# Optimization experiments

Hardware: AMD Instinct MI355X
Metric: run time of the kernel (lower is better)

The kernel has to match this reference:

```python
import math
import jax, jax.numpy as jnp
import numpy as np

N_HEAD = 16
ROPE_BASE = 10000.0


def _rope_tables(T, half, dtype):
    # build_sin_cos(seq_len, dim=head_dim//2): inv freq of length `half`
    pos = jnp.arange(T, dtype=jnp.float32)[:, None]                       # (T,1)
    inv = jnp.exp(jnp.arange(0, 2 * half, 2, dtype=jnp.float32) * (-math.log(ROPE_BASE) / (2 * half)))
    ang = pos * inv                                                        # (T, half)
    return jnp.sin(ang).astype(dtype), jnp.cos(ang).astype(dtype)


def _apply_rope(q, k, sin, cos):
    # q,k: (B,T,H,Dh); sin,cos: (T, Dh//2) -> broadcast over batch and heads
    half = q.shape[-1] // 2
    s = sin[None, :, None, :]
    c = cos[None, :, None, :]
    q1, q2 = q[..., :half], q[..., half:]
    k1, k2 = k[..., :half], k[..., half:]
    q = jnp.concatenate([q1 * c - q2 * s, q2 * c + q1 * s], axis=-1)
    k = jnp.concatenate([k1 * c - k2 * s, k2 * c + k1 * s], axis=-1)
    return q, k


def setup_inputs() -> dict:
    key = jax.random.key(0)
    k1, k2, k3 = jax.random.split(key, 3)
    B, T, C = 2, 2048, 2048
    x = jax.random.normal(k1, (B, T, C), dtype=jnp.float32)
    w_qkv = jax.random.normal(k2, (3 * C, C), dtype=jnp.float32) * (1.0 / math.sqrt(C))
    w_proj = jax.random.normal(k3, (C, C), dtype=jnp.float32) * (1.0 / math.sqrt(C))
    return {"x": x, "w_qkv": w_qkv, "w_proj": w_proj}


def reference(x, w_qkv, w_proj):
    B, T, C = x.shape
    H = N_HEAD
    Dh = C // H
    # fused QKV projection (Linear, no bias): (B,T,3C) -> (B,T,3,H,Dh)
    qkv = jnp.einsum('btc,oc->bto', x, w_qkv).reshape(B, T, 3, H, Dh)
    q, k, v = qkv[:, :, 0], qkv[:, :, 1], qkv[:, :, 2]          # (B,T,H,Dh)
    sin, cos = _rope_tables(T, Dh // 2, x.dtype)
    q, k = _apply_rope(q, k, sin, cos)
    # causal attention, scale 1/sqrt(Dh) (flash default softmax_scale=None)
    scale = 1.0 / math.sqrt(Dh)
    scores = jnp.einsum('bqhd,bkhd->bhqk', q, k) * scale        # (B,H,T,T)
    mask = jnp.tril(jnp.ones((T, T), dtype=bool))
    scores = jnp.where(mask[None, None], scores, jnp.finfo(scores.dtype).min)
    probs = jax.nn.softmax(scores, axis=-1)
    out = jnp.einsum('bhqk,bkhd->bqhd', probs, v)               # (B,T,H,Dh)
    # faithful to original: permute(0,2,1,3) then reshape_as(x)
    out = jnp.transpose(out, (0, 2, 1, 3)).reshape(B, T, C)
    return jnp.einsum('btc,oc->bto', out, w_proj)
```

## Files before the change

kernel.cpp:

```cpp
#include <hip/hip_runtime.h>
#include <hip/hip_bf16.h>

typedef __bf16 bf16_t;
typedef __bf16 bf16x8 __attribute__((ext_vector_type(8)));
typedef float f32x4 __attribute__((ext_vector_type(4)));

#define MFMA16(a, b, c) __builtin_amdgcn_mfma_f32_16x16x32_bf16(a, b, c, 0, 0, 0)

__device__ __forceinline__ void async_copy16(const void* g, void* l) {
  __builtin_amdgcn_global_load_lds(
      (const __attribute__((address_space(1))) void*)g,
      (__attribute__((address_space(3))) void*)l, 16, 0, 0);
}

__global__ void cast_f32_bf16(const float* __restrict__ in, bf16_t* __restrict__ out, int n8) {
  int stride = gridDim.x * blockDim.x;
  for (int i = blockIdx.x * blockDim.x + threadIdx.x; i < n8; i += stride) {
    const float* p = in + (size_t)i * 8;
    f32x4 a = *(const f32x4*)p;
    f32x4 b = *(const f32x4*)(p + 4);
    bf16x8 o;
    o[0] = (bf16_t)a[0]; o[1] = (bf16_t)a[1]; o[2] = (bf16_t)a[2]; o[3] = (bf16_t)a[3];
    o[4] = (bf16_t)b[0]; o[5] = (bf16_t)b[1]; o[6] = (bf16_t)b[2]; o[7] = (bf16_t)b[3];
    *(bf16x8*)(out + (size_t)i * 8) = o;
  }
}

__global__ __launch_bounds__(512, 2) void gemm_qkv(
    const bf16_t* __restrict__ A, const bf16_t* __restrict__ Bw,
    bf16_t* __restrict__ qo, bf16_t* __restrict__ ko,
    int K) {
  __shared__ __align__(16) char lds[131072];
  int tid = threadIdx.x;
  int w = tid >> 6, lane = tid & 63;
  int wm = w & 1, wn = w >> 1;
  int mr = lane & 15, kg = lane >> 4;

  int orig = blockIdx.x;
  int chunk = orig & 7, i = orig >> 3;
  int by = (chunk & 3) * 4 + (i & 3);
  int bx = (chunk >> 2) * 8 + (i >> 2);
  int row0 = by * 256, col0 = bx * 256;

  int lr = tid >> 3, ch = (tid & 7) ^ (lr & 7);
  size_t aoff[4], boff[4];
#pragma unroll
  for (int g = 0; g < 4; ++g) {
    int gr = g * 32 + (lr & 31) + (lr >> 5) * 128;
    aoff[g] = (size_t)(row0 + gr) * K + ch * 8;
  }
#pragma unroll
  for (int p = 0; p < 4; ++p) {
    int gr = (lr >> 4) * 64 + p * 16 + (lr & 15);
    boff[p] = (size_t)(col0 + gr) * K + ch * 8;
  }

  auto stgA = [&](int q, int g, int kt) {
    async_copy16(A + aoff[g] + kt * 64, lds + q * 65536 + g * 8192 + tid * 16);
  };
  auto stgB = [&](int q, int p, int kt) {
    async_copy16(Bw + boff[p] + kt * 64, lds + q * 65536 + 32768 + p * 8192 + tid * 16);
  };

  f32x4 zero = {0.f, 0.f, 0.f, 0.f};
  f32x4 acc[8][4];
#pragma unroll
  for (int mi = 0; mi < 8; ++mi)
#pragma unroll
    for (int ni = 0; ni < 4; ++ni) acc[mi][ni] = zero;

  int nt = K >> 6;

  stgB(0, 0, 0); stgB(0, 1, 0); stgB(0, 2, 0); stgB(0, 3, 0);
  stgA(0, 0, 0); stgA(0, 1, 0); stgA(0, 2, 0); stgA(0, 3, 0);
  asm volatile("s_waitcnt vmcnt(0)" ::: "memory");
  __builtin_amdgcn_sched_barrier(0);
  __builtin_amdgcn_s_barrier();
  __builtin_amdgcn_sched_barrier(0);

#pragma unroll 1
  for (int t = 0; t < nt; ++t) {
    int q = t & 1, qn = q ^ 1;
    int kt = (t + 1 < nt) ? (t + 1) : t;
    const char* Ab = lds + q * 65536;
    const char* Bb = Ab + 32768;
    bf16x8 bf[4][2];

#define QKV_PHASE(MI0, STG0, STG1, WAIT)                                        \
    {                                                                           \
      int r0 = ((MI0) >> 1) * 64 + wm * 32 + mr;                                \
      int r1 = r0 + 16;                                                         \
      bf16x8 a00 = *(const bf16x8*)(Ab + r0 * 128 + ((kg * 16) ^ ((r0 & 7) << 4)));      \
      bf16x8 a01 = *(const bf16x8*)(Ab + r0 * 128 + ((64 + kg * 16) ^ ((r0 & 7) << 4))); \
      bf16x8 a10 = *(const bf16x8*)(Ab + r1 * 128 + ((kg * 16) ^ ((r1 & 7) << 4)));      \
      bf16x8 a11 = *(const bf16x8*)(Ab + r1 * 128 + ((64 + kg * 16) ^ ((r1 & 7) << 4))); \
      STG0; STG1;                                                               \
      __builtin_amdgcn_sched_barrier(0);                                        \
      asm volatile("s_waitcnt vmcnt(" #WAIT ")" ::: "memory");                  \
      __builtin_amdgcn_s_barrier();                                             \
      asm volatile("s_waitcnt lgkmcnt(0)" ::: "memory");                        \
      __builtin_amdgcn_sched_barrier(0);                                        \
      __builtin_amdgcn_s_setprio(1);                                            \
      _Pragma("unroll")                                                         \
      for (int ni = 0; ni < 4; ++ni) {                                          \
        acc[MI0][ni] = MFMA16(a00, bf[ni][0], acc[MI0][ni]);                    \
        acc[MI0][ni] = MFMA16(a01, bf[ni][1], acc[MI0][ni]);                    \
        acc[(MI0) + 1][ni] = MFMA16(a10, bf[ni][0], acc[(MI0) + 1][ni]);        \
        acc[(MI0) + 1][ni] = MFMA16(a11, bf[ni][1], acc[(MI0) + 1][ni]);        \
      }                                                                         \
      __builtin_amdgcn_s_setprio(0);                                            \
      __builtin_amdgcn_sched_barrier(0);                                        \
      __builtin_amdgcn_s_barrier();                                             \
      __builtin_amdgcn_sched_barrier(0);                                        \
    }

#pragma unroll
    for (int ni = 0; ni < 4; ++ni) {
      int rb = ni * 64 + wn * 16 + mr;
      bf[ni][0] = *(const bf16x8*)(Bb + rb * 128 + ((kg * 16) ^ ((rb & 7) << 4)));
      bf[ni][1] = *(const bf16x8*)(Bb + rb * 128 + ((64 + kg * 16) ^ ((rb & 7) << 4)));
    }
    QKV_PHASE(0, stgB(qn, 0, kt), stgB(qn, 1, kt), 4)
    QKV_PHASE(2, stgB(qn, 2, kt), stgB(qn, 3, kt), 5)
    QKV_PHASE(4, stgA(qn, 0, kt), stgA(qn, 1, kt), 6)
    QKV_PHASE(6, stgA(qn, 2, kt), stgA(qn, 3, kt), 3)
#undef QKV_PHASE
  }
  asm volatile("s_waitcnt vmcnt(0)" ::: "memory");
  __syncthreads();

  char* tb = &lds[0];
  int s = col0 >> 11;
  int h0 = (col0 >> 7) & 15;
  int b = row0 >> 11, t0 = row0 & 2047;
#pragma unroll
  for (int mi = 0; mi < 8; ++mi)
#pragma unroll
    for (int ni = 0; ni < 4; ++ni)
#pragma unroll
      for (int jj = 0; jj < 4; ++jj) {
        int rl = wm * 128 + mi * 16 + kg * 4 + jj;
        int cb = (wn * 64 + ni * 16 + mr) * 2;
        *(bf16_t*)(tb + rl * 512 + (cb ^ ((rl & 7) << 4))) = (bf16_t)acc[mi][ni][jj];
      }
  __syncthreads();
  int r = tid >> 1, hs = tid & 1;
  const char* rowb = tb + r * 512;
  int sz = (r & 7) << 4;
  int t = t0 + r;
  bf16_t* dst = (s == 0 ? qo : ko) + ((size_t)((b * 16 + h0 + hs) * 2048 + t)) * 128;
  float tf = (float)t;
  const float cinv = -0.20762050593046014f;
  float postm = (s == 0) ? 0.12751744f : 1.0f;
  bf16x8 vin[16];
#pragma unroll
  for (int m = 0; m < 16; ++m)
    vin[m] = *(const bf16x8*)(rowb + ((hs * 256 + m * 16) ^ sz));
#pragma unroll
  for (int m = 0; m < 8; ++m) {
    bf16x8 o1, o2;
#pragma unroll
    for (int e = 0; e < 8; ++e) {
      float ang = tf * exp2f((float)(m * 8 + e) * cinv);
      float sv = __sinf(ang), cv = __cosf(ang);
      float x1 = (float)vin[m][e], x2 = (float)vin[m + 8][e];
      o1[e] = (bf16_t)((x1 * cv - x2 * sv) * postm);
      o2[e] = (bf16_t)((x2 * cv + x1 * sv) * postm);
    }
    *(bf16x8*)(dst + m * 8) = o1;
    *(bf16x8*)(dst + 64 + m * 8) = o2;
  }
}

template <int MODE>
__global__ __launch_bounds__(512, 2) void gemm256(
    const bf16_t* __restrict__ A, const bf16_t* __restrict__ Bw, float* __restrict__ C,
    bf16_t* __restrict__ vto, int M, int N, int K, int nby, int colbase) {
  __shared__ __align__(16) char lds[147456];
  int tid = threadIdx.x;
  int w = tid >> 6, lane = tid & 63;
  int wm = w >> 1, wn = w & 1;
  int mr = lane & 15, kg = lane >> 4;

  int nwg = gridDim.x;
  int orig = blockIdx.x;
  int wgid = (orig & 7) * (nwg >> 3) + (orig >> 3);
  int by = wgid % nby, bx = wgid / nby;
  int row0 = by * 256, col0 = colbase + bx * 128;

  size_t aoff[4], boff[2];
#pragma unroll
  for (int it = 0; it < 4; ++it) {
    int c = tid + it * 512;
    int r = c >> 3;
    int chs = (c & 7) ^ (r & 7);
    aoff[it] = (size_t)(row0 + r) * K + chs * 8;
  }
#pragma unroll
  for (int it = 0; it < 2; ++it) {
    int c = tid + it * 512;
    int r = c >> 3;
    int chs = (c & 7) ^ (r & 7);
    boff[it] = (size_t)(col0 - colbase + r) * K + chs * 8;
  }

  auto stageA = [&](int buf, int kt, int half) {
    char* Ad = &lds[buf * 49152];
#pragma unroll
    for (int it = half * 2; it < half * 2 + 2; ++it)
      async_copy16(A + aoff[it] + kt * 64, Ad + (tid + it * 512) * 16);
  };
  auto stageB = [&](int buf, int kt) {
    char* Bd = &lds[buf * 49152 + 32768];
#pragma unroll
    for (int it = 0; it < 2; ++it)
      async_copy16(Bw + boff[it] + kt * 64, Bd + (tid + it * 512) * 16);
  };

  f32x4 zero = {0.f, 0.f, 0.f, 0.f};
  f32x4 acc[4][4];
#pragma unroll
  for (int mi = 0; mi < 4; ++mi)
#pragma unroll
    for (int ni = 0; ni < 4; ++ni) acc[mi][ni] = zero;

  int nt = K >> 6;
  stageA(0, 0, 0); stageA(0, 0, 1); stageB(0, 0);
  stageA(1, 1, 0); stageA(1, 1, 1); stageB(1, 1);
  asm volatile("s_waitcnt vmcnt(6)" ::: "memory");
  __builtin_amdgcn_sched_barrier(0);
  __builtin_amdgcn_s_barrier();
  __builtin_amdgcn_sched_barrier(0);

#pragma unroll 1
  for (int t = 0; t < nt; ++t) {
    int cur = t % 3;
    int nxt = (t + 2) % 3;
    int kt2 = (t + 2 < nt) ? (t + 2) : t;
    const char* Ab = &lds[cur * 49152];
    const char* Bb = &lds[cur * 49152 + 32768];
    bf16x8 af[4][2], bfr[4][2];
#pragma unroll
    for (int mi = 0; mi < 4; ++mi) {
      int row = wm * 64 + mi * 16 + mr;
      const char* rb = Ab + row * 128;
      int sz = (row & 7) << 4;
      af[mi][0] = *(const bf16x8*)(rb + ((kg * 16) ^ sz));
      af[mi][1] = *(const bf16x8*)(rb + ((64 + kg * 16) ^ sz));
    }
#pragma unroll
    for (int ni = 0; ni < 4; ++ni) {
      int row = wn * 64 + ni * 16 + mr;
      const char* rb = Bb + row * 128;
      int sz = (row & 7) << 4;
      bfr[ni][0] = *(const bf16x8*)(rb + ((kg * 16) ^ sz));
      bfr[ni][1] = *(const bf16x8*)(rb + ((64 + kg * 16) ^ sz));
    }
    stageA(nxt, kt2, 0);
    __builtin_amdgcn_s_setprio(1);
#pragma unroll
    for (int mi = 0; mi < 4; ++mi) {
      acc[mi][0] = MFMA16(af[mi][0], bfr[0][0], acc[mi][0]);
      acc[mi][0] = MFMA16(af[mi][1], bfr[0][1], acc[mi][0]);
    }
    __builtin_amdgcn_s_setprio(0);
    stageA(nxt, kt2, 1);
    __builtin_amdgcn_s_setprio(1);
#pragma unroll
    for (int mi = 0; mi < 4; ++mi) {
      acc[mi][1] = MFMA16(af[mi][0], bfr[1][0], acc[mi][1]);
      acc[mi][1] = MFMA16(af[mi][1], bfr[1][1], acc[mi][1]);
    }
    __builtin_amdgcn_s_setprio(0);
    stageB(nxt, kt2);
    __builtin_amdgcn_s_setprio(1);
#pragma unroll
    for (int mi = 0; mi < 4; ++mi) {
      acc[mi][2] = MFMA16(af[mi][0], bfr[2][0], acc[mi][2]);
      acc[mi][2] = MFMA16(af[mi][1], bfr[2][1], acc[mi][2]);
      acc[mi][3] = MFMA16(af[mi][0], bfr[3][0], acc[mi][3]);
      acc[mi][3] = MFMA16(af[mi][1], bfr[3][1], acc[mi][3]);
    }
    __builtin_amdgcn_s_setprio(0);
    asm volatile("s_waitcnt vmcnt(6)" ::: "memory");
    __builtin_amdgcn_sched_barrier(0);
    __builtin_amdgcn_s_barrier();
    __builtin_amdgcn_sched_barrier(0);
  }
  asm volatile("s_waitcnt vmcnt(0)" ::: "memory");
  __syncthreads();

  if (MODE == 0) {
#pragma unroll
    for (int mi = 0; mi < 4; ++mi)
#pragma unroll
      for (int ni = 0; ni < 4; ++ni)
#pragma unroll
        for (int jj = 0; jj < 4; ++jj) {
          int row = row0 + wm * 64 + mi * 16 + kg * 4 + jj;
          int col = col0 + wn * 64 + ni * 16 + mr;
          C[(size_t)row * N + col] = acc[mi][ni][jj];
        }
  } else {
    char* tb = &lds[0];
    int h = (col0 >> 7) & 15;
    int b = row0 >> 11, t0 = row0 & 2047;
#pragma unroll
    for (int mi = 0; mi < 4; ++mi)
#pragma unroll
      for (int ni = 0; ni < 4; ++ni)
#pragma unroll
        for (int jj = 0; jj < 4; ++jj) {
          int rloc = wm * 64 + mi * 16 + kg * 4 + jj;
          int cloc = wn * 64 + ni * 16 + mr;
          *(bf16_t*)(tb + cloc * 512 + ((rloc * 2) ^ ((cloc & 7) << 4))) =
              (bf16_t)acc[mi][ni][jj];
        }
    __syncthreads();
    int d = tid >> 2, qt = tid & 3;
    const char* rowb = tb + d * 512;
    int sz = (d & 7) << 4;
    bf16_t* dst = vto + ((size_t)((b * 16 + h) * 128 + d)) * 2048 + t0 + qt * 64;
#pragma unroll
    for (int m2 = 0; m2 < 8; ++m2)
      *(bf16x8*)(dst + m2 * 8) = *(const bf16x8*)(rowb + ((qt * 128 + m2 * 16) ^ sz));
  }
}

__global__ __launch_bounds__(256, 4) void attn_kernel(
    const bf16_t* __restrict__ qg, const bf16_t* __restrict__ kgl,
    const bf16_t* __restrict__ vtg, bf16_t* __restrict__ og) {
  __shared__ __align__(16) bf16_t Ks[64 * 128];
  __shared__ __align__(16) bf16_t Vs[128 * 64];
  __shared__ __align__(16) bf16_t plds[4][1024];
  const int T = 2048;
  int tid = threadIdx.x;
  int w = tid >> 6, lane = tid & 63;
  int mr = lane & 15, kg = lane >> 4;
  int swz = (mr & 7) << 4;

  int L = blockIdx.x;
  int xcd = L & 7, idx = L >> 3;
  int bh = xcd * 4 + (idx & 3);
  int qb = 31 - (idx >> 2);

  const bf16_t* Q = qg + (size_t)bh * T * 128;
  const bf16_t* K = kgl + (size_t)bh * T * 128;
  const bf16_t* Vt = vtg + (size_t)bh * 128 * T;

  int sb = tid * 16;
  int krl = sb >> 8;
  int kc = (sb & 255) ^ ((krl & 7) << 4);
  size_t ksrc = (size_t)krl * 128 + (kc >> 1);
  int vdl = sb >> 7;
  int vc = (sb & 127) ^ ((vdl & 7) << 4);
  size_t vsrc = (size_t)vdl * 2048 + (vc >> 1);

  auto stage = [&](int kb) {
#pragma unroll
    for (int it = 0; it < 4; ++it)
      async_copy16(K + (size_t)(kb + it * 16) * 128 + ksrc, &Ks[it * 2048 + tid * 8]);
#pragma unroll
    for (int it = 0; it < 4; ++it)
      async_copy16(Vt + (size_t)it * 65536 + kb + vsrc, &Vs[it * 2048 + tid * 8]);
  };

  f32x4 zero = {0.f, 0.f, 0.f, 0.f};
  bf16_t* P = &plds[w][0];
  int b = bh >> 4, h = bh & 15;

  int qr0 = qb * 64 + w * 16;
  bf16x8 qf[4];
#pragma unroll
  for (int db = 0; db < 4; ++db)
    qf[db] = *(const bf16x8*)(Q + (size_t)(qr0 + mr) * 128 + db * 32 + kg * 8);

  f32x4 acc[8];
#pragma unroll
  for (int d2 = 0; d2 < 8; ++d2) acc[d2] = zero;
  float mrun[4] = {-1e30f, -1e30f, -1e30f, -1e30f};
  float lpart[4] = {0.f, 0.f, 0.f, 0.f};

  int nj = qb + 1;
#pragma unroll 1
  for (int j = 0; j < nj; ++j) {
    __syncthreads();
    stage(j * 64);
    asm volatile("s_waitcnt vmcnt(0)" ::: "memory");
    __builtin_amdgcn_sched_barrier(0);
    __syncthreads();
    const char* KsB = (const char*)&Ks[0];
    const char* VsB = (const char*)&Vs[0];
    int kb = j * 64;
    f32x4 s[4];
    __builtin_amdgcn_s_setprio(1);
#pragma unroll
    for (int ntl = 0; ntl < 4; ++ntl) {
      s[ntl] = zero;
      int rowb = (ntl * 16 + mr) * 256;
#pragma unroll
      for (int db = 0; db < 4; ++db) {
        bf16x8 kf = *(const bf16x8*)(KsB + rowb + ((db * 64 + kg * 16) ^ swz));
        s[ntl] = MFMA16(qf[db], kf, s[ntl]);
      }
    }
    __builtin_amdgcn_s_setprio(0);
    float pvv[4][4];
    float lmax[4] = {-3e38f, -3e38f, -3e38f, -3e38f};
    bool diag = (j == qb);
#pragma unroll
    for (int ntl = 0; ntl < 4; ++ntl)
#pragma unroll
      for (int jj = 0; jj < 4; ++jj) {
        float v = s[ntl][jj];
        if (diag && (kb + ntl * 16 + mr) > (qr0 + kg * 4 + jj)) v = -1e30f;
        pvv[ntl][jj] = v;
        lmax[jj] = fmaxf(lmax[jj], v);
      }
    bool ok = true;
#pragma unroll
    for (int jj = 0; jj < 4; ++jj) ok &= (lmax[jj] <= mrun[jj] + 8.0f);
    if (!__all(ok)) {
      float tmax[4];
#pragma unroll
      for (int jj = 0; jj < 4; ++jj) tmax[jj] = lmax[jj];
#pragma unroll
      for (int m = 1; m < 16; m <<= 1)
#pragma unroll
        for (int jj = 0; jj < 4; ++jj)
          tmax[jj] = fmaxf(tmax[jj], __shfl_xor(tmax[jj], m, 64));
#pragma unroll
      for (int jj = 0; jj < 4; ++jj) {
        float mn = fmaxf(mrun[jj], tmax[jj]);
        float corr = __builtin_amdgcn_exp2f(mrun[jj] - mn);
        mrun[jj] = mn;
        lpart[jj] *= corr;
#pragma unroll
        for (int d2 = 0; d2 < 8; ++d2) acc[d2][jj] *= corr;
      }
    }
#pragma unroll
    for (int ntl = 0; ntl < 4; ++ntl)
#pragma unroll
      for (int jj = 0; jj < 4; ++jj) {
        float p = __builtin_amdgcn_exp2f(pvv[ntl][jj] - mrun[jj]);
        pvv[ntl][jj] = p;
        lpart[jj] += p;
      }
#pragma unroll
    for (int ntl = 0; ntl < 4; ++ntl)
#pragma unroll
      for (int jj = 0; jj < 4; ++jj) {
        int rr = kg * 4 + jj;
        int cbyte = (mr + ntl * 16) * 2;
        *(bf16_t*)((char*)P + rr * 128 + (cbyte ^ ((rr & 7) << 4))) = (bf16_t)pvv[ntl][jj];
      }
    __builtin_amdgcn_s_setprio(1);
#pragma unroll
    for (int ks = 0; ks < 2; ++ks) {
      int cb = (ks * 32 + kg * 8) * 2;
      bf16x8 pa = *(const bf16x8*)((const char*)P + mr * 128 + (cb ^ ((mr & 7) << 4)));
#pragma unroll
      for (int d2 = 0; d2 < 8; ++d2) {
        bf16x8 vf = *(const bf16x8*)(VsB + (d2 * 16 + mr) * 128 + ((ks * 64 + kg * 16) ^ swz));
        acc[d2] = MFMA16(pa, vf, acc[d2]);
      }
    }
    __builtin_amdgcn_s_setprio(0);
  }
#pragma unroll
  for (int m = 1; m < 16; m <<= 1)
#pragma unroll
    for (int jj = 0; jj < 4; ++jj) lpart[jj] += __shfl_xor(lpart[jj], m, 64);
#pragma unroll
  for (int jj = 0; jj < 4; ++jj) {
    float invl = 1.0f / lpart[jj];
    int t = qr0 + kg * 4 + jj;
    size_t row = (size_t)b * 2048 + h * 128 + (t >> 4);
    bf16_t* orow = og + row * 2048 + (t & 15) * 128;
#pragma unroll
    for (int d2 = 0; d2 < 8; ++d2)
      orow[d2 * 16 + mr] = (bf16_t)(acc[d2][jj] * invl);
  }
}

extern "C" void kernel_launch(void* const* d_in, const int* in_sizes, int n_in,
                              void* d_out, int out_size, void* d_ws, size_t ws_size,
                              hipStream_t stream) {
  const float* x = (const float*)d_in[0];
  const float* wqkv = (const float*)d_in[1];
  const float* wproj = (const float*)d_in[2];
  float* out = (float*)d_out;
  char* ws = (char*)d_ws;

  const size_t OFF_WQKV = 16777216;
  const size_t OFF_Q = 41943040;
  const size_t OFF_K = 58720256;
  const size_t OFF_VT = 75497472;

  bf16_t* xb = (bf16_t*)(ws);
  bf16_t* wqkvb = (bf16_t*)(ws + OFF_WQKV);
  bf16_t* g_q = (bf16_t*)(ws + OFF_Q);
  bf16_t* g_k = (bf16_t*)(ws + OFF_K);
  bf16_t* g_vt = (bf16_t*)(ws + OFF_VT);
  bf16_t* g_att = (bf16_t*)(ws);
  bf16_t* wprojb = (bf16_t*)(ws + OFF_WQKV);

  cast_f32_bf16<<<2048, 256, 0, stream>>>(x, xb, 8388608 / 8);
  cast_f32_bf16<<<2048, 256, 0, stream>>>(wqkv, wqkvb, 12582912 / 8);
  gemm_qkv<<<256, 512, 0, stream>>>(xb, wqkvb, g_q, g_k, 2048);
  gemm256<1><<<256, 512, 0, stream>>>(xb, wqkvb + (size_t)4096 * 2048, nullptr, g_vt,
                                      4096, 2048, 2048, 16, 4096);
  cast_f32_bf16<<<2048, 256, 0, stream>>>(wproj, wprojb, 4194304 / 8);
  attn_kernel<<<1024, 256, 0, stream>>>(g_q, g_k, g_vt, g_att);
  gemm256<0><<<256, 512, 0, stream>>>(g_att, wprojb, out, nullptr, 4096, 2048, 2048, 16, 0);
}
```

Measured before the change: 247.0 us.

## Double-buffer K/V in attention, use 128-row q blocks with paired causal tiles

The attention kernel moves to 512-thread blocks covering 128 query rows. K/V tiles are double-buffered so the next tile's async global-to-LDS copy overlaps compute. Each block handles two q-blocks (bx and 15-bx) so every block does the same causal work, and the grid shrinks to 256 blocks. The cost is twice the LDS, fewer resident blocks per CU, and 256 blocks that may not fill all CUs.

```diff
diff --git a/kernel.cpp b/kernel.cpp
--- a/kernel.cpp
+++ b/kernel.cpp
@@ -327,12 +327,12 @@
   }
 }
 
-__global__ __launch_bounds__(256, 4) void attn_kernel(
+__global__ __launch_bounds__(512, 2) void attn_kernel(
     const bf16_t* __restrict__ qg, const bf16_t* __restrict__ kgl,
     const bf16_t* __restrict__ vtg, bf16_t* __restrict__ og) {
-  __shared__ __align__(16) bf16_t Ks[64 * 128];
-  __shared__ __align__(16) bf16_t Vs[128 * 64];
-  __shared__ __align__(16) bf16_t plds[4][1024];
+  __shared__ __align__(16) bf16_t Ks[2][64 * 128];
+  __shared__ __align__(16) bf16_t Vs[2][128 * 64];
+  __shared__ __align__(16) bf16_t plds[8][1024];
   const int T = 2048;
   int tid = threadIdx.x;
   int w = tid >> 6, lane = tid & 63;
@@ -340,147 +340,163 @@
   int swz = (mr & 7) << 4;
 
   int L = blockIdx.x;
-  int xcd = L & 7, idx = L >> 3;
-  int bh = xcd * 4 + (idx & 3);
-  int qb = 31 - (idx >> 2);
+  int role = (L & 7) * 32 + (L >> 3);
+  int bx = role & 7, bh = role >> 3;
 
   const bf16_t* Q = qg + (size_t)bh * T * 128;
   const bf16_t* K = kgl + (size_t)bh * T * 128;
   const bf16_t* Vt = vtg + (size_t)bh * 128 * T;
 
-  int sb = tid * 16;
-  int krl = sb >> 8;
-  int kc = (sb & 255) ^ ((krl & 7) << 4);
-  size_t ksrc = (size_t)krl * 128 + (kc >> 1);
-  int vdl = sb >> 7;
-  int vc = (sb & 127) ^ ((vdl & 7) << 4);
-  size_t vsrc = (size_t)vdl * 2048 + (vc >> 1);
-
-  auto stage = [&](int kb) {
-#pragma unroll
-    for (int it = 0; it < 4; ++it)
-      async_copy16(K + (size_t)(kb + it * 16) * 128 + ksrc, &Ks[it * 2048 + tid * 8]);
-#pragma unroll
-    for (int it = 0; it < 4; ++it)
-      async_copy16(Vt + (size_t)it * 65536 + kb + vsrc, &Vs[it * 2048 + tid * 8]);
+  size_t ksrc[2], vsrc[2];
+#pragma unroll
+  for (int it = 0; it < 2; ++it) {
+    int c = it * 512 + tid;
+    int sb = c * 16;
+    int krl = sb >> 8;
+    int kc = (sb & 255) ^ ((krl & 7) << 4);
+    ksrc[it] = (size_t)krl * 128 + (kc >> 1);
+    int vdl = sb >> 7;
+    int vc = (sb & 127) ^ ((vdl & 7) << 4);
+    vsrc[it] = (size_t)vdl * 2048 + (vc >> 1);
+  }
+
+  auto stage = [&](int buf, int kb) {
+#pragma unroll
+    for (int it = 0; it < 2; ++it)
+      async_copy16(K + (size_t)kb * 128 + ksrc[it], &Ks[buf][(it * 512 + tid) * 8]);
+#pragma unroll
+    for (int it = 0; it < 2; ++it)
+      async_copy16(Vt + kb + vsrc[it], &Vs[buf][(it * 512 + tid) * 8]);
   };
 
   f32x4 zero = {0.f, 0.f, 0.f, 0.f};
   bf16_t* P = &plds[w][0];
   int b = bh >> 4, h = bh & 15;
 
-  int qr0 = qb * 64 + w * 16;
-  bf16x8 qf[4];
-#pragma unroll
-  for (int db = 0; db < 4; ++db)
-    qf[db] = *(const bf16x8*)(Q + (size_t)(qr0 + mr) * 128 + db * 32 + kg * 8);
-
-  f32x4 acc[8];
-#pragma unroll
-  for (int d2 = 0; d2 < 8; ++d2) acc[d2] = zero;
-  float mrun[4] = {-1e30f, -1e30f, -1e30f, -1e30f};
-  float lpart[4] = {0.f, 0.f, 0.f, 0.f};
-
-  int nj = qb + 1;
 #pragma unroll 1
-  for (int j = 0; j < nj; ++j) {
+  for (int pp = 0; pp < 2; ++pp) {
+    int qb = pp ? bx : (15 - bx);
+    int qr0 = qb * 128 + w * 16;
+    bf16x8 qf[4];
+#pragma unroll
+    for (int db = 0; db < 4; ++db)
+      qf[db] = *(const bf16x8*)(Q + (size_t)(qr0 + mr) * 128 + db * 32 + kg * 8);
+
+    f32x4 acc[8];
+#pragma unroll
+    for (int d2 = 0; d2 < 8; ++d2) acc[d2] = zero;
+    float mrun[4] = {-1e30f, -1e30f, -1e30f, -1e30f};
+    float lpart[4] = {0.f, 0.f, 0.f, 0.f};
+
+    int nj = 2 * qb + 2;
     __syncthreads();
-    stage(j * 64);
-    asm volatile("s_waitcnt vmcnt(0)" ::: "memory");
-    __builtin_amdgcn_sched_barrier(0);
-    __syncthreads();
-    const char* KsB = (const char*)&Ks[0];
-    const char* VsB = (const char*)&Vs[0];
-    int kb = j * 64;
-    f32x4 s[4];
-    __builtin_amdgcn_s_setprio(1);
-#pragma unroll
-    for (int ntl = 0; ntl < 4; ++ntl) {
-      s[ntl] = zero;
-      int rowb = (ntl * 16 + mr) * 256;
-#pragma unroll
-      for (int db = 0; db < 4; ++db) {
-        bf16x8 kf = *(const bf16x8*)(KsB + rowb + ((db * 64 + kg * 16) ^ swz));
-        s[ntl] = MFMA16(qf[db], kf, s[ntl]);
+    stage(0, 0);
+    if (nj > 1) stage(1, 64);
+#pragma unroll 1
+    for (int j = 0; j < nj; ++j) {
+      int cur = j & 1;
+      if (j + 1 < nj) {
+        asm volatile("s_waitcnt vmcnt(4)" ::: "memory");
+      } else {
+        asm volatile("s_waitcnt vmcnt(0)" ::: "memory");
       }
-    }
-    __builtin_amdgcn_s_setprio(0);
-    float pvv[4][4];
-    float lmax[4] = {-3e38f, -3e38f, -3e38f, -3e38f};
-    bool diag = (j == qb);
-#pragma unroll
-    for (int ntl = 0; ntl < 4; ++ntl)
-#pragma unroll
-      for (int jj = 0; jj < 4; ++jj) {
-        float v = s[ntl][jj];
-        if (diag && (kb + ntl * 16 + mr) > (qr0 + kg * 4 + jj)) v = -1e30f;
-        pvv[ntl][jj] = v;
-        lmax[jj] = fmaxf(lmax[jj], v);
+      __builtin_amdgcn_sched_barrier(0);
+      __syncthreads();
+      const char* KsB = (const char*)&Ks[cur][0];
+      const char* VsB = (const char*)&Vs[cur][0];
+      int kb = j * 64;
+      f32x4 s[4];
+      __builtin_amdgcn_s_setprio(1);
+#pragma unroll
+      for (int ntl = 0; ntl < 4; ++ntl) {
+        s[ntl] = zero;
+        int rowb = (ntl * 16 + mr) * 256;
+#pragma unroll
+        for (int db = 0; db < 4; ++db) {
+          bf16x8 kf = *(const bf16x8*)(KsB + rowb + ((db * 64 + kg * 16) ^ swz));
+          s[ntl] = MFMA16(qf[db], kf, s[ntl]);
+        }
       }
-    bool ok = true;
-#pragma unroll
-    for (int jj = 0; jj < 4; ++jj) ok &= (lmax[jj] <= mrun[jj] + 8.0f);
-    if (!__all(ok)) {
-      float tmax[4];
-#pragma unroll
-      for (int jj = 0; jj < 4; ++jj) tmax[jj] = lmax[jj];
-#pragma unroll
-      for (int m = 1; m < 16; m <<= 1)
-#pragma unroll
-        for (int jj = 0; jj < 4; ++jj)
-          tmax[jj] = fmaxf(tmax[jj], __shfl_xor(tmax[jj], m, 64));
-#pragma unroll
-      for (int jj = 0; jj < 4; ++jj) {
-        float mn = fmaxf(mrun[jj], tmax[jj]);
-        float corr = __builtin_amdgcn_exp2f(mrun[jj] - mn);
-        mrun[jj] = mn;
-        lpart[jj] *= corr;
-#pragma unroll
-        for (int d2 = 0; d2 < 8; ++d2) acc[d2][jj] *= corr;
+      __builtin_amdgcn_s_setprio(0);
+      float pvv[4][4];
+      float lmax[4] = {-3e38f, -3e38f, -3e38f, -3e38f};
+      bool diag = (kb + 63 > qr0);
+#pragma unroll
+      for (int ntl = 0; ntl < 4; ++ntl)
+#pragma unroll
+        for (int jj = 0; jj < 4; ++jj) {
+          float v = s[ntl][jj];
+          if (diag && (kb + ntl * 16 + mr) > (qr0 + kg * 4 + jj)) v = -1e30f;
+          pvv[ntl][jj] = v;
+          lmax[jj] = fmaxf(lmax[jj], v);
+        }
+      bool ok = true;
+#pragma unroll
+      for (int jj = 0; jj < 4; ++jj) ok &= (lmax[jj] <= mrun[jj] + 8.0f);
+      if (!__all(ok)) {
+        float tmax[4];
+#pragma unroll
+        for (int jj = 0; jj < 4; ++jj) tmax[jj] = lmax[jj];
+#pragma unroll
+        for (int m = 1; m < 16; m <<= 1)
+#pragma unroll
+          for (int jj = 0; jj < 4; ++jj)
+            tmax[jj] = fmaxf(tmax[jj], __shfl_xor(tmax[jj], m, 64));
+#pragma unroll
+        for (int jj = 0; jj < 4; ++jj) {
+          float mn = fmaxf(mrun[jj], tmax[jj]);
+          float corr = __builtin_amdgcn_exp2f(mrun[jj] - mn);
+          mrun[jj] = mn;
+          lpart[jj] *= corr;
+#pragma unroll
+          for (int d2 = 0; d2 < 8; ++d2) acc[d2][jj] *= corr;
+        }
       }
-    }
-#pragma unroll
-    for (int ntl = 0; ntl < 4; ++ntl)
-#pragma unroll
-      for (int jj = 0; jj < 4; ++jj) {
-        float p = __builtin_amdgcn_exp2f(pvv[ntl][jj] - mrun[jj]);
-        pvv[ntl][jj] = p;
-        lpart[jj] += p;
+#pragma unroll
+      for (int ntl = 0; ntl < 4; ++ntl)
+#pragma unroll
+        for (int jj = 0; jj < 4; ++jj) {
+          float p = __builtin_amdgcn_exp2f(pvv[ntl][jj] - mrun[jj]);
+          pvv[ntl][jj] = p;
+          lpart[jj] += p;
+        }
+#pragma unroll
+      for (int ntl = 0; ntl < 4; ++ntl)
+#pragma unroll
+        for (int jj = 0; jj < 4; ++jj) {
+          int rr = kg * 4 + jj;
+          int cbyte = (mr + ntl * 16) * 2;
+          *(bf16_t*)((char*)P + rr * 128 + (cbyte ^ ((rr & 7) << 4))) = (bf16_t)pvv[ntl][jj];
+        }
+      __builtin_amdgcn_s_setprio(1);
+#pragma unroll
+      for (int ks = 0; ks < 2; ++ks) {
+        int cb = (ks * 32 + kg * 8) * 2;
+        bf16x8 pa = *(const bf16x8*)((const char*)P + mr * 128 + (cb ^ ((mr & 7) << 4)));
+#pragma unroll
+        for (int d2 = 0; d2 < 8; ++d2) {
+          bf16x8 vf = *(const bf16x8*)(VsB + (d2 * 16 + mr) * 128 + ((ks * 64 + kg * 16) ^ swz));
+          acc[d2] = MFMA16(pa, vf, acc[d2]);
+        }
       }
-#pragma unroll
-    for (int ntl = 0; ntl < 4; ++ntl)
-#pragma unroll
-      for (int jj = 0; jj < 4; ++jj) {
-        int rr = kg * 4 + jj;
-        int cbyte = (mr + ntl * 16) * 2;
-        *(bf16_t*)((char*)P + rr * 128 + (cbyte ^ ((rr & 7) << 4))) = (bf16_t)pvv[ntl][jj];
-      }
-    __builtin_amdgcn_s_setprio(1);
-#pragma unroll
-    for (int ks = 0; ks < 2; ++ks) {
-      int cb = (ks * 32 + kg * 8) * 2;
-      bf16x8 pa = *(const bf16x8*)((const char*)P + mr * 128 + (cb ^ ((mr & 7) << 4)));
-#pragma unroll
-      for (int d2 = 0; d2 < 8; ++d2) {
-        bf16x8 vf = *(const bf16x8*)(VsB + (d2 * 16 + mr) * 128 + ((ks * 64 + kg * 16) ^ swz));
-        acc[d2] = MFMA16(pa, vf, acc[d2]);
-      }
-    }
-    __builtin_amdgcn_s_setprio(0);
-  }
-#pragma unroll
-  for (int m = 1; m < 16; m <<= 1)
-#pragma unroll
-    for (int jj = 0; jj < 4; ++jj) lpart[jj] += __shfl_xor(lpart[jj], m, 64);
-#pragma unroll
-  for (int jj = 0; jj < 4; ++jj) {
-    float invl = 1.0f / lpart[jj];
-    int t = qr0 + kg * 4 + jj;
-    size_t row = (size_t)b * 2048 + h * 128 + (t >> 4);
-    bf16_t* orow = og + row * 2048 + (t & 15) * 128;
-#pragma unroll
-    for (int d2 = 0; d2 < 8; ++d2)
-      orow[d2 * 16 + mr] = (bf16_t)(acc[d2][jj] * invl);
+      __builtin_amdgcn_s_setprio(0);
+      __syncthreads();
+      if (j + 2 < nj) stage(cur, (j + 2) * 64);
+    }
+#pragma unroll
+    for (int m = 1; m < 16; m <<= 1)
+#pragma unroll
+      for (int jj = 0; jj < 4; ++jj) lpart[jj] += __shfl_xor(lpart[jj], m, 64);
+#pragma unroll
+    for (int jj = 0; jj < 4; ++jj) {
+      float invl = 1.0f / lpart[jj];
+      int t = qr0 + kg * 4 + jj;
+      size_t row = (size_t)b * 2048 + h * 128 + (t >> 4);
+      bf16_t* orow = og + row * 2048 + (t & 15) * 128;
+#pragma unroll
+      for (int d2 = 0; d2 < 8; ++d2)
+        orow[d2 * 16 + mr] = (bf16_t)(acc[d2][jj] * invl);
+    }
   }
 }
 
@@ -512,6 +528,6 @@
   gemm256<1><<<256, 512, 0, stream>>>(xb, wqkvb + (size_t)4096 * 2048, nullptr, g_vt,
                                       4096, 2048, 2048, 16, 4096);
   cast_f32_bf16<<<2048, 256, 0, stream>>>(wproj, wprojb, 4194304 / 8);
-  attn_kernel<<<1024, 256, 0, stream>>>(g_q, g_k, g_vt, g_att);
+  attn_kernel<<<256, 512, 0, stream>>>(g_q, g_k, g_vt, g_att);
   gemm256<0><<<256, 512, 0, stream>>>(g_att, wprojb, out, nullptr, 4096, 2048, 2048, 16, 0);
 }
```

After: 249.6 us. No clear change (+1.1%).
